# Performance work log

Measured on AMD Instinct MI355X. Metric: run time of the kernel, lower is better.

The kernel has to match this reference:

```python
import jax, jax.numpy as jnp
import numpy as np

DIM = 768
HEADS = 12
HEAD_DIM = DIM // HEADS
HIDDEN = int(DIM * 4.0)
EPS = 1e-5
SCALE = HEAD_DIM ** -0.5


def _layernorm(x, g, b):
    m = jnp.mean(x, axis=-1, keepdims=True)
    v = jnp.mean(jnp.square(x - m), axis=-1, keepdims=True)
    return (x - m) * jax.lax.rsqrt(v + EPS) * g + b


def setup_inputs() -> dict:
    key = jax.random.key(0)
    ks = jax.random.split(key, 12)
    B, N = 2, 2048
    s = 0.02
    return {
        "x": jax.random.normal(ks[0], (B, N, DIM), dtype=jnp.float32),
        "mask": jax.random.randint(ks[1], (B, N), 0, 2, dtype=jnp.int32),
        "ln1_g": jnp.ones((DIM,), jnp.float32),
        "ln1_b": jnp.zeros((DIM,), jnp.float32),
        "qkv_w": jax.random.normal(ks[2], (3 * DIM, DIM), jnp.float32) * s,
        "proj_w": jax.random.normal(ks[3], (DIM, DIM), jnp.float32) * s,
        "proj_b": jnp.zeros((DIM,), jnp.float32),
        "ln2_g": jnp.ones((DIM,), jnp.float32),
        "ln2_b": jnp.zeros((DIM,), jnp.float32),
        "fc1_w": jax.random.normal(ks[4], (HIDDEN, DIM), jnp.float32) * s,
        "fc1_b": jnp.zeros((HIDDEN,), jnp.float32),
        "fc2_w": jax.random.normal(ks[5], (DIM, HIDDEN), jnp.float32) * s,
        "fc2_b": jnp.zeros((DIM,), jnp.float32),
    }


def reference(x, mask, ln1_g, ln1_b, qkv_w, proj_w, proj_b, ln2_g, ln2_b,
              fc1_w, fc1_b, fc2_w, fc2_b):
    B, N, C = x.shape
    # --- attention on norm1(x) ---
    h = _layernorm(x, ln1_g, ln1_b)
    qkv = (h @ qkv_w.T).reshape(B, N, 3, HEADS, HEAD_DIM)
    q, k, v = qkv[:, :, 0], qkv[:, :, 1], qkv[:, :, 2]  # [B,N,H,D]
    scores = jnp.einsum('bnhd,bmhd->bhnm', q, k) * SCALE  # [B,H,N,N]
    neg_inf = jnp.finfo(scores.dtype).min
    scores = jnp.where(mask[:, None, None, :] == 1, neg_inf, scores)
    attn = jax.nn.softmax(scores, axis=-1)
    y = jnp.einsum('bhnm,bmhd->bnhd', attn, v).reshape(B, N, C)
    y = y @ proj_w.T + proj_b
    x = x + y
    # --- MLP on norm2(x) ---
    h2 = _layernorm(x, ln2_g, ln2_b)
    h2 = jax.nn.gelu(h2 @ fc1_w.T + fc1_b, approximate=False)
    x = x + (h2 @ fc2_w.T + fc2_b)
    return x
```

## Files before the change

kernel.cpp:

```cpp
#include <hip/hip_runtime.h>
#include <math.h>
#include <float.h>

#define DIM 768
#define HEADS 12
#define HD 64
#define HIDDEN 3072
#define SEQ 2048
#define BATCH 2
#define NTOK (BATCH * SEQ)
#define QKVC (3 * DIM)
#define LN_EPS 1e-5f
#define SC2 0.1803368801111f

typedef unsigned short u16;
typedef __attribute__((ext_vector_type(8))) __bf16 bf16x8;
typedef __attribute__((ext_vector_type(8))) unsigned short u16x8;
typedef __attribute__((ext_vector_type(4))) float f32x4;

__device__ __forceinline__ u16 f2bf(float f) {
    unsigned int u = __builtin_bit_cast(unsigned int, f);
    u += 0x7fffu + ((u >> 16) & 1u);
    return (u16)(u >> 16);
}

__device__ __forceinline__ f32x4 mfma16(u16x8 a, u16x8 b, f32x4 c) {
    return __builtin_amdgcn_mfma_f32_16x16x32_bf16(
        __builtin_bit_cast(bf16x8, a), __builtin_bit_cast(bf16x8, b), c, 0, 0, 0);
}

__device__ __forceinline__ void gl2lds16(const void* g, void* l) {
    __builtin_amdgcn_global_load_lds(
        (const __attribute__((address_space(1))) void*)g,
        (__attribute__((address_space(3))) void*)l, 16, 0, 0);
}

__device__ __forceinline__ float gelu_f(float v) {
    return 0.5f * v * (1.0f + erff(v * 0.70710678118654752f));
}

__global__ __launch_bounds__(256) void cvt_all(const float* __restrict__ qkvw,
                                               const float* __restrict__ projw,
                                               const float* __restrict__ fc1w,
                                               const float* __restrict__ fc2w,
                                               u16* __restrict__ o_qkv,
                                               u16* __restrict__ o_proj,
                                               u16* __restrict__ o_fc1,
                                               u16* __restrict__ o_fc2) {
    long i = (long)(blockIdx.x * 256 + threadIdx.x) * 4;
    const float* s; u16* d; long off;
    if (i < 1769472)      { s = qkvw;  d = o_qkv;  off = i; }
    else if (i < 2359296) { s = projw; d = o_proj; off = i - 1769472; }
    else if (i < 4718592) { s = fc1w;  d = o_fc1;  off = i - 2359296; }
    else                  { s = fc2w;  d = o_fc2;  off = i - 4718592; }
    float4 v = *(const float4*)(s + off);
    ushort4 o;
    o.x = f2bf(v.x); o.y = f2bf(v.y); o.z = f2bf(v.z); o.w = f2bf(v.w);
    *(ushort4*)(d + off) = o;
}

__global__ __launch_bounds__(256) void scan_mask(const int* __restrict__ mask,
                                                 int* __restrict__ pos,
                                                 int* __restrict__ cnt,
                                                 float* __restrict__ cbias) {
    int b = blockIdx.x, t = threadIdx.x;
    const int* m = mask + b * SEQ;
    int v[8], s = 0;
#pragma unroll
    for (int j = 0; j < 8; ++j) { v[j] = (m[t * 8 + j] == 1) ? 0 : 1; s += v[j]; }
    __shared__ int red[256];
    __shared__ int tot;
    red[t] = s;
    __syncthreads();
    for (int off = 1; off < 256; off <<= 1) {
        int x = (t >= off) ? red[t - off] : 0;
        __syncthreads();
        red[t] += x;
        __syncthreads();
    }
    int base = red[t] - s;
    if (t == 255) tot = red[255];
    __syncthreads();
#pragma unroll
    for (int j = 0; j < 8; ++j) {
        pos[b * SEQ + t * 8 + j] = v[j] ? base : -1;
        base += v[j];
    }
    if (t == 0) cnt[b] = tot;
#pragma unroll
    for (int j = 0; j < 8; ++j) {
        int idx = t * 8 + j;
        cbias[b * SEQ + idx] = (idx < tot) ? 0.0f : -1e30f;
    }
}

__global__ __launch_bounds__(256) void ln_kernel(const float* __restrict__ x,
                                                 const float* __restrict__ g,
                                                 const float* __restrict__ bta,
                                                 u16* __restrict__ out) {
    int row = blockIdx.x;
    int t = threadIdx.x;
    const float* xr = x + (size_t)row * DIM;
    float v0 = xr[t], v1 = xr[t + 256], v2 = xr[t + 512];
    __shared__ float red[256];
    red[t] = v0 + v1 + v2;
    __syncthreads();
    for (int off = 128; off > 0; off >>= 1) {
        if (t < off) red[t] += red[t + off];
        __syncthreads();
    }
    float mean = red[0] * (1.0f / DIM);
    __syncthreads();
    float d0 = v0 - mean, d1 = v1 - mean, d2 = v2 - mean;
    red[t] = d0 * d0 + d1 * d1 + d2 * d2;
    __syncthreads();
    for (int off = 128; off > 0; off >>= 1) {
        if (t < off) red[t] += red[t + off];
        __syncthreads();
    }
    float rstd = rsqrtf(red[0] * (1.0f / DIM) + LN_EPS);
    u16* orow = out + (size_t)row * DIM;
    orow[t]       = f2bf(d0 * rstd * g[t]       + bta[t]);
    orow[t + 256] = f2bf(d1 * rstd * g[t + 256] + bta[t + 256]);
    orow[t + 512] = f2bf(d2 * rstd * g[t + 512] + bta[t + 512]);
}

__global__ __launch_bounds__(256) void repack_kv(const u16* __restrict__ qkv,
                                                 const int* __restrict__ pos,
                                                 u16* __restrict__ kh,
                                                 u16* __restrict__ vth) {
    int s = blockIdx.x;
    int bh = blockIdx.y;
    int b = bh / HEADS, h = bh % HEADS;
    int t = threadIdx.x;
    __shared__ u16 Vl[64 * 72];
    __shared__ int lpos[64];
    const u16* base = qkv + ((size_t)(b * SEQ + s * 64)) * QKVC + h * HD;
    if (t < 64) lpos[t] = pos[b * SEQ + s * 64 + t];
    {
        int vkey = (t & 31) * 2, vd0 = (t >> 5) * 8;
        const u16* g0 = base + 2 * DIM + (size_t)vkey * QKVC + vd0;
        u16x8 a = *(const u16x8*)g0;
        u16x8 c = *(const u16x8*)(g0 + QKVC);
#pragma unroll
        for (int j = 0; j < 8; ++j) {
            unsigned int pk = (unsigned int)a[j] | ((unsigned int)c[j] << 16);
            *(unsigned int*)(Vl + (vd0 + j) * 72 + vkey) = pk;
        }
    }
    __syncthreads();
    {
        int r = t >> 2, d0 = (t & 3) * 16;
        int p = lpos[r];
        if (p >= 0) {
            const u16* g = base + DIM + (size_t)r * QKVC + d0;
            u16* o = kh + (size_t)bh * (SEQ * HD) + (size_t)p * HD + d0;
            *(uint4*)o = *(const uint4*)g;
            *(uint4*)(o + 8) = *(const uint4*)(g + 8);
        }
    }
    {
        int d = t >> 2, m0 = (t & 3) * 16;
        u16* orow = vth + (size_t)bh * (HD * SEQ) + (size_t)d * SEQ;
#pragma unroll
        for (int j = 0; j < 16; ++j) {
            int p = lpos[m0 + j];
            if (p >= 0) orow[p] = Vl[d * 72 + m0 + j];
        }
    }
}

template <int BM, int BN, int EPI>
__global__ __launch_bounds__(256) void mgemm(const u16* __restrict__ A,
                                             const u16* __restrict__ Bw,
                                             void* __restrict__ Cout,
                                             int N, int K,
                                             const float* __restrict__ bias,
                                             const float* __restrict__ resid) {
    constexpr int WM = BM / 2, WN = BN / 2, NI = WM / 16, NJ = WN / 16;
    constexpr int ACALLS = (BM * 64) / 4096;
    constexpr int BCALLS = (BN * 64) / 4096;
    __shared__ u16 As[BM * 32];
    __shared__ u16 Bs[BN * 32];
    int t = threadIdx.x;
    int w = t >> 6, lane = t & 63;
    int quad = lane >> 4, m16 = lane & 15;
    int row0 = blockIdx.y * BM, col0 = blockIdx.x * BN;
    int lrow = lane >> 2;
    int lkb = (lane & 3) * 16;

    f32x4 acc[NI][NJ] = {};

    for (int k0 = 0; k0 < K; k0 += 32) {
        __syncthreads();
#pragma unroll
        for (int c = 0; c < ACALLS; ++c) {
            int off = (w * ACALLS + c) * 1024;
            int r = (off >> 6) + lrow;
            const u16* g = A + (size_t)(row0 + r) * K + k0 + (lkb >> 1);
            gl2lds16(g, As + (off >> 1));
        }
#pragma unroll
        for (int c = 0; c < BCALLS; ++c) {
            int off = (w * BCALLS + c) * 1024;
            int r = (off >> 6) + lrow;
            const u16* g = Bw + (size_t)(col0 + r) * K + k0 + (lkb >> 1);
            gl2lds16(g, Bs + (off >> 1));
        }
        __syncthreads();
        u16x8 af[NI], bfj[NJ];
#pragma unroll
        for (int i = 0; i < NI; ++i)
            af[i] = *(const u16x8*)(As + ((w >> 1) * WM + 16 * i + m16) * 32 + quad * 8);
#pragma unroll
        for (int j = 0; j < NJ; ++j)
            bfj[j] = *(const u16x8*)(Bs + ((w & 1) * WN + 16 * j + m16) * 32 + quad * 8);
#pragma unroll
        for (int i = 0; i < NI; ++i)
#pragma unroll
            for (int j = 0; j < NJ; ++j)
                acc[i][j] = mfma16(af[i], bfj[j], acc[i][j]);
    }

    int wr0 = row0 + (w >> 1) * WM, wc0 = col0 + (w & 1) * WN;
#pragma unroll
    for (int i = 0; i < NI; ++i)
#pragma unroll
        for (int j = 0; j < NJ; ++j) {
            int ccol = wc0 + 16 * j + m16;
#pragma unroll
            for (int r = 0; r < 4; ++r) {
                int crow = wr0 + 16 * i + quad * 4 + r;
                float v = acc[i][j][r];
                if (EPI == 0) {
                    ((u16*)Cout)[(size_t)crow * N + ccol] = f2bf(v);
                } else if (EPI == 1) {
                    v += bias[ccol] + resid[(size_t)crow * N + ccol];
                    ((float*)Cout)[(size_t)crow * N + ccol] = v;
                } else {
                    v = gelu_f(v + bias[ccol]);
                    ((u16*)Cout)[(size_t)crow * N + ccol] = f2bf(v);
                }
            }
        }
}

__global__ __launch_bounds__(256, 3) void attn_mfma(const u16* __restrict__ qkv,
                                                    const u16* __restrict__ kh,
                                                    const u16* __restrict__ vth,
                                                    const float* __restrict__ cbias,
                                                    const int* __restrict__ cnt,
                                                    u16* __restrict__ y) {
    int qt = blockIdx.x, bh = blockIdx.y;
    int b = bh / HEADS, h = bh % HEADS;
    int t = threadIdx.x, w = t >> 6, lane = t & 63;
    int quad = lane >> 4, m16 = lane & 15;
    __shared__ u16 Ks[128 * 64];
    __shared__ u16 Vt[64 * 128];
    __shared__ u16 Pw[4][16 * 136];
    const u16* kbase = kh + (size_t)bh * (SEQ * HD);
    const u16* vbase = vth + (size_t)bh * (SEQ * HD);
    const float* mrow = cbias + b * SEQ;

    int qrow = b * SEQ + qt * 64 + w * 16 + m16;
    const u16* qp = qkv + (size_t)qrow * QKVC + h * HD + quad * 8;
    u16x8 qf0 = *(const u16x8*)qp;
    u16x8 qf1 = *(const u16x8*)(qp + 32);

    int rloc = lane >> 3, kslot = lane & 7;
    int kchunk = kslot ^ rloc;
    int dloc = lane >> 4, vslot = lane & 15;

    float mrun[4], lrun[4];
    f32x4 O[4] = {};
#pragma unroll
    for (int r = 0; r < 4; ++r) { mrun[r] = -3e38f; lrun[r] = 0.f; }

    int slo = quad ^ (m16 & 7);

    int cntb = cnt[b];
    int ntile = (cntb + 127) >> 7;

    for (int kt = 0; kt < ntile; ++kt) {
        int k0 = kt << 7;
        __syncthreads();
#pragma unroll
        for (int c = 0; c < 4; ++c) {
            int rb = (w * 4 + c) * 8;
            const u16* g = kbase + (size_t)(k0 + rb + rloc) * HD + kchunk * 8;
            gl2lds16(g, Ks + (w * 4 + c) * 512);
        }
#pragma unroll
        for (int c = 0; c < 4; ++c) {
            int d = (w * 4 + c) * 4 + dloc;
            int chunk = vslot ^ (d & 15);
            const u16* g = vbase + (size_t)d * SEQ + k0 + chunk * 8;
            gl2lds16(g, Vt + (w * 4 + c) * 512);
        }
        float kb[8];
#pragma unroll
        for (int nb = 0; nb < 8; ++nb) kb[nb] = mrow[k0 + m16 + 16 * nb];
        __syncthreads();

        float sv[8][4];
#pragma unroll
        for (int nb = 0; nb < 8; ++nb) {
            const u16* krow = Ks + (m16 + 16 * nb) * 64;
            f32x4 s = {0.f, 0.f, 0.f, 0.f};
            s = mfma16(qf0, *(const u16x8*)(krow + slo * 8), s);
            s = mfma16(qf1, *(const u16x8*)(krow + (slo ^ 4) * 8), s);
#pragma unroll
            for (int r = 0; r < 4; ++r) sv[nb][r] = s[r] * SC2 + kb[nb];
        }
        float tmax[4];
#pragma unroll
        for (int r = 0; r < 4; ++r) {
            float a0 = fmaxf(fmaxf(sv[0][r], sv[1][r]), fmaxf(sv[2][r], sv[3][r]));
            float a1 = fmaxf(fmaxf(sv[4][r], sv[5][r]), fmaxf(sv[6][r], sv[7][r]));
            tmax[r] = fmaxf(a0, a1);
        }
#pragma unroll
        for (int off = 1; off < 16; off <<= 1)
#pragma unroll
            for (int r = 0; r < 4; ++r)
                tmax[r] = fmaxf(tmax[r], __shfl_xor(tmax[r], off));
        float al[4], ps[4];
#pragma unroll
        for (int r = 0; r < 4; ++r) {
            float mn = fmaxf(mrun[r], tmax[r]);
            al[r] = __builtin_amdgcn_exp2f(mrun[r] - mn);
            mrun[r] = mn;
            ps[r] = 0.f;
        }
#pragma unroll
        for (int nb = 0; nb < 8; ++nb)
#pragma unroll
            for (int r = 0; r < 4; ++r) {
                float p = __builtin_amdgcn_exp2f(sv[nb][r] - mrun[r]);
                sv[nb][r] = p;
                ps[r] += p;
            }
#pragma unroll
        for (int off = 1; off < 16; off <<= 1)
#pragma unroll
            for (int r = 0; r < 4; ++r)
                ps[r] += __shfl_xor(ps[r], off);
#pragma unroll
        for (int r = 0; r < 4; ++r) lrun[r] = lrun[r] * al[r] + ps[r];
#pragma unroll
        for (int nbd = 0; nbd < 4; ++nbd)
#pragma unroll
            for (int r = 0; r < 4; ++r) O[nbd][r] *= al[r];
#pragma unroll
        for (int nb = 0; nb < 8; ++nb)
#pragma unroll
            for (int r = 0; r < 4; ++r)
                Pw[w][(quad * 4 + r) * 136 + m16 + 16 * nb] = f2bf(sv[nb][r]);
        u16x8 pf[4];
#pragma unroll
        for (int ks = 0; ks < 4; ++ks)
            pf[ks] = *(const u16x8*)(Pw[w] + m16 * 136 + ks * 32 + quad * 8);
#pragma unroll
        for (int nbd = 0; nbd < 4; ++nbd) {
            const u16* vrow = Vt + (nbd * 16 + m16) * 128;
#pragma unroll
            for (int ks = 0; ks < 4; ++ks) {
                int sl = (quad + 4 * ks) ^ m16;
                O[nbd] = mfma16(pf[ks], *(const u16x8*)(vrow + sl * 8), O[nbd]);
            }
        }
    }
#pragma unroll
    for (int r = 0; r < 4; ++r) {
        float inv = 1.0f / lrun[r];
        int tok = b * SEQ + qt * 64 + w * 16 + quad * 4 + r;
        u16* yr = y + (size_t)tok * DIM + h * HD + m16;
#pragma unroll
        for (int nbd = 0; nbd < 4; ++nbd) yr[16 * nbd] = f2bf(O[nbd][r] * inv);
    }
}

extern "C" void kernel_launch(void* const* d_in, const int* in_sizes, int n_in,
                              void* d_out, int out_size, void* d_ws, size_t ws_size,
                              hipStream_t stream) {
    const float* x      = (const float*)d_in[0];
    const int*   mask   = (const int*)d_in[1];
    const float* ln1_g  = (const float*)d_in[2];
    const float* ln1_b  = (const float*)d_in[3];
    const float* qkv_w  = (const float*)d_in[4];
    const float* proj_w = (const float*)d_in[5];
    const float* proj_b = (const float*)d_in[6];
    const float* ln2_g  = (const float*)d_in[7];
    const float* ln2_b  = (const float*)d_in[8];
    const float* fc1_w  = (const float*)d_in[9];
    const float* fc1_b  = (const float*)d_in[10];
    const float* fc2_w  = (const float*)d_in[11];
    const float* fc2_b  = (const float*)d_in[12];
    float* out = (float*)d_out;

    char* W = (char*)d_ws;
    u16*   wqkv  = (u16*)(W + 0);
    u16*   wproj = (u16*)(W + 3538944);
    u16*   wfc1  = (u16*)(W + 4718592);
    u16*   wfc2  = (u16*)(W + 9437184);
    u16*   hbuf  = (u16*)(W + 14155776);
    float* x1    = (float*)(W + 20447232);
    float* cbias = (float*)(W + 20447232);
    int*   posb  = (int*)(W + 20463616);
    int*   cntb  = (int*)(W + 20480000);
    u16*   qkvb  = (u16*)(W + 33030144);
    u16*   ybuf  = (u16*)(W + 51904512);
    u16*   a1    = (u16*)(W + 33030144);
    u16*   khb   = (u16*)(W + 58212352);
    u16*   vthb  = (u16*)(W + 64503808);

    cvt_all<<<6912, 256, 0, stream>>>(qkv_w, proj_w, fc1_w, fc2_w,
                                      wqkv, wproj, wfc1, wfc2);
    scan_mask<<<BATCH, 256, 0, stream>>>(mask, posb, cntb, cbias);

    ln_kernel<<<NTOK, 256, 0, stream>>>(x, ln1_g, ln1_b, hbuf);
    mgemm<128, 128, 0><<<dim3(QKVC / 128, NTOK / 128), 256, 0, stream>>>(
        hbuf, wqkv, qkvb, QKVC, DIM, nullptr, nullptr);
    repack_kv<<<dim3(SEQ / 64, BATCH * HEADS), 256, 0, stream>>>(qkvb, posb, khb, vthb);
    attn_mfma<<<dim3(SEQ / 64, BATCH * HEADS), 256, 0, stream>>>(
        qkvb, khb, vthb, cbias, cntb, ybuf);
    mgemm<128, 64, 1><<<dim3(DIM / 64, NTOK / 128), 256, 0, stream>>>(
        ybuf, wproj, x1, DIM, DIM, proj_b, x);
    ln_kernel<<<NTOK, 256, 0, stream>>>(x1, ln2_g, ln2_b, hbuf);
    mgemm<128, 128, 2><<<dim3(HIDDEN / 128, NTOK / 128), 256, 0, stream>>>(
        hbuf, wfc1, a1, HIDDEN, DIM, fc1_b, nullptr);
    mgemm<128, 64, 1><<<dim3(DIM / 64, NTOK / 128), 256, 0, stream>>>(
        a1, wfc2, out, DIM, HIDDEN, fc2_b, x1);
}
```

Baseline: 317.4 us.

## Split-K the fc2 GEMM and remap block order for cache locality

The fc2 GEMM (K=3072, only 384 tiles) is split into two K halves along grid z. One half writes fp32 partials to scratch and the other writes to the output, then a merge kernel adds the partials, bias and residual. Block indices in the GEMMs and attention are also remapped into groups of 8 along y so that concurrently running blocks share operand tiles in L2. This adds an extra merge pass and roughly 12 MB more fp32 traffic in exchange for more parallelism on the long-K GEMM.

```diff
diff --git a/kernel.cpp b/kernel.cpp
--- a/kernel.cpp
+++ b/kernel.cpp
@@ -174,7 +174,8 @@
 __global__ __launch_bounds__(256) void mgemm(const u16* __restrict__ A,
                                              const u16* __restrict__ Bw,
                                              void* __restrict__ Cout,
-                                             int N, int K,
+                                             void* __restrict__ Cout2,
+                                             int N, int klen,
                                              const float* __restrict__ bias,
                                              const float* __restrict__ resid) {
     constexpr int WM = BM / 2, WN = BN / 2, NI = WM / 16, NJ = WN / 16;
@@ -185,13 +186,19 @@
     int t = threadIdx.x;
     int w = t >> 6, lane = t & 63;
     int quad = lane >> 4, m16 = lane & 15;
-    int row0 = blockIdx.y * BM, col0 = blockIdx.x * BN;
+    int gx = gridDim.x;
+    int flat = blockIdx.y * gx + blockIdx.x;
+    int bx = (flat >> 3) % gx;
+    int by = (flat & 7) + 8 * ((flat >> 3) / gx);
+    int K = klen * gridDim.z;
+    int kbeg = blockIdx.z * klen, kend = kbeg + klen;
+    int row0 = by * BM, col0 = bx * BN;
     int lrow = lane >> 2;
     int lkb = (lane & 3) * 16;
 
     f32x4 acc[NI][NJ] = {};
 
-    for (int k0 = 0; k0 < K; k0 += 32) {
+    for (int k0 = kbeg; k0 < kend; k0 += 32) {
         __syncthreads();
 #pragma unroll
         for (int c = 0; c < ACALLS; ++c) {
@@ -222,6 +229,7 @@
                 acc[i][j] = mfma16(af[i], bfj[j], acc[i][j]);
     }
 
+    void* dst = blockIdx.z ? Cout2 : Cout;
     int wr0 = row0 + (w >> 1) * WM, wc0 = col0 + (w & 1) * WN;
 #pragma unroll
     for (int i = 0; i < NI; ++i)
@@ -233,16 +241,33 @@
                 int crow = wr0 + 16 * i + quad * 4 + r;
                 float v = acc[i][j][r];
                 if (EPI == 0) {
-                    ((u16*)Cout)[(size_t)crow * N + ccol] = f2bf(v);
+                    ((u16*)dst)[(size_t)crow * N + ccol] = f2bf(v);
                 } else if (EPI == 1) {
                     v += bias[ccol] + resid[(size_t)crow * N + ccol];
-                    ((float*)Cout)[(size_t)crow * N + ccol] = v;
+                    ((float*)dst)[(size_t)crow * N + ccol] = v;
+                } else if (EPI == 2) {
+                    v = gelu_f(v + bias[ccol]);
+                    ((u16*)dst)[(size_t)crow * N + ccol] = f2bf(v);
                 } else {
-                    v = gelu_f(v + bias[ccol]);
-                    ((u16*)Cout)[(size_t)crow * N + ccol] = f2bf(v);
+                    ((float*)dst)[(size_t)crow * N + ccol] = v;
                 }
             }
         }
+}
+
+__global__ __launch_bounds__(256) void merge_kernel(float* __restrict__ out,
+                                                    const float* __restrict__ part,
+                                                    const float* __restrict__ bias,
+                                                    const float* __restrict__ resid) {
+    int i = (blockIdx.x * 256 + threadIdx.x) * 4;
+    int col = i % DIM;
+    float4 o = *(const float4*)(out + i);
+    float4 p = *(const float4*)(part + i);
+    float4 rr = *(const float4*)(resid + i);
+    float4 bb = *(const float4*)(bias + col);
+    o.x += p.x + rr.x + bb.x; o.y += p.y + rr.y + bb.y;
+    o.z += p.z + rr.z + bb.z; o.w += p.w + rr.w + bb.w;
+    *(float4*)(out + i) = o;
 }
 
 __global__ __launch_bounds__(256, 3) void attn_mfma(const u16* __restrict__ qkv,
@@ -251,7 +276,10 @@
                                                     const float* __restrict__ cbias,
                                                     const int* __restrict__ cnt,
                                                     u16* __restrict__ y) {
-    int qt = blockIdx.x, bh = blockIdx.y;
+    int gx = gridDim.x;
+    int flat = blockIdx.y * gx + blockIdx.x;
+    int qt = (flat >> 3) % gx;
+    int bh = (flat & 7) + 8 * ((flat >> 3) / gx);
     int b = bh / HEADS, h = bh % HEADS;
     int t = threadIdx.x, w = t >> 6, lane = t & 63;
     int quad = lane >> 4, m16 = lane & 15;
@@ -413,6 +441,7 @@
     u16*   a1    = (u16*)(W + 33030144);
     u16*   khb   = (u16*)(W + 58212352);
     u16*   vthb  = (u16*)(W + 64503808);
+    float* pp    = (float*)(W + 58212352);
 
     cvt_all<<<6912, 256, 0, stream>>>(qkv_w, proj_w, fc1_w, fc2_w,
                                       wqkv, wproj, wfc1, wfc2);
@@ -420,15 +449,16 @@
 
     ln_kernel<<<NTOK, 256, 0, stream>>>(x, ln1_g, ln1_b, hbuf);
     mgemm<128, 128, 0><<<dim3(QKVC / 128, NTOK / 128), 256, 0, stream>>>(
-        hbuf, wqkv, qkvb, QKVC, DIM, nullptr, nullptr);
+        hbuf, wqkv, qkvb, nullptr, QKVC, DIM, nullptr, nullptr);
     repack_kv<<<dim3(SEQ / 64, BATCH * HEADS), 256, 0, stream>>>(qkvb, posb, khb, vthb);
     attn_mfma<<<dim3(SEQ / 64, BATCH * HEADS), 256, 0, stream>>>(
         qkvb, khb, vthb, cbias, cntb, ybuf);
     mgemm<128, 64, 1><<<dim3(DIM / 64, NTOK / 128), 256, 0, stream>>>(
-        ybuf, wproj, x1, DIM, DIM, proj_b, x);
+        ybuf, wproj, x1, nullptr, DIM, DIM, proj_b, x);
     ln_kernel<<<NTOK, 256, 0, stream>>>(x1, ln2_g, ln2_b, hbuf);
     mgemm<128, 128, 2><<<dim3(HIDDEN / 128, NTOK / 128), 256, 0, stream>>>(
-        hbuf, wfc1, a1, HIDDEN, DIM, fc1_b, nullptr);
-    mgemm<128, 64, 1><<<dim3(DIM / 64, NTOK / 128), 256, 0, stream>>>(
-        a1, wfc2, out, DIM, HIDDEN, fc2_b, x1);
-}
+        hbuf, wfc1, a1, nullptr, HIDDEN, DIM, fc1_b, nullptr);
+    mgemm<128, 64, 3><<<dim3(DIM / 64, NTOK / 128, 2), 256, 0, stream>>>(
+        a1, wfc2, pp, out, DIM, HIDDEN / 2, nullptr, nullptr);
+    merge_kernel<<<NTOK * DIM / 1024, 256, 0, stream>>>(out, pp, fc2_b, x1);
+}
```

New measurement: 307.0 us. 3.3% less time.
